# Kernel tuning notes

Hardware: AMD Instinct MI355X
Metric: run time of the kernel (lower is better)

The kernel has to match this reference:

```python
import jax, jax.numpy as jnp
import numpy as np

NH, DH = 16, 64          # n_head, d_head
CH = NH + DH             # 80
RQ, RK, RV = 6, 2, 2
ROPE_BASE = 10000.0


def _rotary(b, cache_len):
    # b: [B, T, R, DH]; rotates the d-factor exactly as the torch Rotary module
    T = b.shape[1]
    inv_freq = (1.0 / ROPE_BASE) ** (jnp.arange(0, DH, 2, dtype=jnp.float32) / DH)
    t = jnp.arange(T, dtype=jnp.float32) + cache_len
    freqs = jnp.outer(t, inv_freq)                      # [T, DH/2]
    cos = freqs[None, :, None, :].astype(b.dtype)
    sin = jnp.sin(freqs)[None, :, None, :].astype(b.dtype)
    cos = jnp.cos(freqs)[None, :, None, :].astype(b.dtype)
    x1, x2 = jnp.split(b, 2, axis=3)
    return jnp.concatenate([x1 * cos + x2 * sin, -x1 * sin + x2 * cos], axis=3)


def setup_inputs() -> dict:
    key = jax.random.key(0)
    k1, k2, k3, k4 = jax.random.split(key, 4)
    B, T, D = 2, 2048, 1024
    x = jax.random.normal(k1, (B, T, D), dtype=jnp.float32)
    # xavier-uniform-like scale for factor projections
    s_q = float(np.sqrt(6.0 / (D + CH)))
    s_o = float(np.sqrt(6.0 / (D + D)))
    W_abq = jax.random.uniform(k2, (RQ * CH, D), minval=-s_q, maxval=s_q, dtype=jnp.float32)
    W_abkv = jax.random.uniform(k3, ((RK + RV) * CH, D), minval=-s_q, maxval=s_q, dtype=jnp.float32)
    W_o = jax.random.uniform(k4, (D, D), minval=-s_o, maxval=s_o, dtype=jnp.float32)
    return {"x": x, "W_abq": W_abq, "W_abkv": W_abkv, "W_o": W_o}


def reference(x, W_abq, W_abkv, W_o):
    B, T, D = x.shape
    # low-rank factor projections
    abq = (x @ W_abq.T).reshape(B, T, RQ, CH)
    a_q, b_q = abq[..., :NH], abq[..., NH:]            # [B,T,RQ,NH], [B,T,RQ,DH]
    abkv = (x @ W_abkv.T).reshape(B, T, RK + RV, CH)
    a_kv = abkv[..., :NH]
    b_kv = _rotary(abkv[..., NH:], cache_len=0)        # RoPE applied to K/V d-factors only
    a_k, b_k = a_kv[:, :, :RK], b_kv[:, :, :RK]
    a_v, b_v = a_kv[:, :, RK:], b_kv[:, :, RK:]
    # tensor-product reconstruction of Q/K/V
    q = jnp.einsum('btrh,btrd->bthd', a_q, b_q) / RQ
    k = jnp.einsum('btrh,btrd->bthd', a_k, b_k) / RK
    v = jnp.einsum('btrh,btrd->bthd', a_v, b_v) / RV
    # causal attention (flex_attention default scale = 1/sqrt(dh))
    scale = 1.0 / jnp.sqrt(jnp.asarray(DH, dtype=q.dtype))
    scores = jnp.einsum('bqhd,bkhd->bhqk', q, k) * scale
    causal = jnp.tril(jnp.ones((T, T), dtype=bool))
    scores = jnp.where(causal[None, None], scores, jnp.finfo(scores.dtype).min)
    attn = jax.nn.softmax(scores, axis=-1)
    y = jnp.einsum('bhqk,bkhd->bqhd', attn, v).reshape(B, T, D)
    return y @ W_o.T
```

## Files before the change

### kernel.cpp

```cpp
#include <hip/hip_runtime.h>
#include <hip/hip_bf16.h>
#include <math.h>

#define NHEADS 16
#define DHEAD  64
#define CHDIM  80
#define RQn    6
#define RKn    2
#define RVn    2
#define BB     2
#define TT     2048
#define DDim   1024
#define NQK    800

using frag16 = __attribute__((ext_vector_type(8))) short;
using f32x4  = __attribute__((ext_vector_type(4))) float;
using f32x16 = __attribute__((ext_vector_type(16))) float;
using uint2v = __attribute__((ext_vector_type(2))) unsigned int;

#define AS1(p) ((const __attribute__((address_space(1))) unsigned int*)(p))
#define AS3(p) ((__attribute__((address_space(3))) unsigned int*)(p))

static __device__ __forceinline__ unsigned short bf16_bits(float f) {
    __hip_bfloat16 h = __float2bfloat16(f);
    return *(unsigned short*)&h;
}
static __device__ __forceinline__ unsigned int pk2(float a, float b) {
    return ((unsigned int)bf16_bits(b) << 16) | (unsigned int)bf16_bits(a);
}
static __device__ __forceinline__ float bfu2f(unsigned short u) {
    return __uint_as_float(((unsigned int)u) << 16);
}
static __device__ __forceinline__ float exp2_hw(float x) {
    return __builtin_amdgcn_exp2f(x);
}

__global__ __launch_bounds__(256) void cvt_all(
    const float* __restrict__ x, const float* __restrict__ wq,
    const float* __restrict__ wk, const float* __restrict__ wo,
    __hip_bfloat16* __restrict__ xb, __hip_bfloat16* __restrict__ wqk,
    __hip_bfloat16* __restrict__ wob)
{
    int bid = blockIdx.x;
    const float* src; __hip_bfloat16* dst; int n4;
    if (bid < 4096)      { src = x;  dst = xb;            n4 = 1048576; }
    else if (bid < 4576) { bid -= 4096; src = wq; dst = wqk;           n4 = 122880; }
    else if (bid < 4896) { bid -= 4576; src = wk; dst = wqk + 491520;  n4 = 81920; }
    else                 { bid -= 4896; src = wo; dst = wob;           n4 = 262144; }
    int i = bid * 256 + threadIdx.x;
    if (i < n4) {
        float4 v = *(const float4*)&src[i * 4];
        ushort4 o;
        o.x = bf16_bits(v.x); o.y = bf16_bits(v.y);
        o.z = bf16_bits(v.z); o.w = bf16_bits(v.w);
        *(ushort4*)&dst[i * 4] = o;
    }
}

template <bool BF16OUT>
__global__ __launch_bounds__(256) void gemm_bf16(
    const __hip_bfloat16* __restrict__ A, const __hip_bfloat16* __restrict__ W,
    void* __restrict__ Cv, int M, int N, int K)
{
    __shared__ __hip_bfloat16 Asl[2][64 * 64];
    __shared__ __hip_bfloat16 Bsl[2][128 * 64];
    const int tid = threadIdx.x;
    const int w = tid >> 6, lane = tid & 63;
    const int l16 = lane & 15, quad = lane >> 4;
    const int bm = blockIdx.y * 64, bn = blockIdx.x * 128;

    int rSA[2], cSA[2];
    #pragma unroll
    for (int j = 0; j < 2; j++) {
        int L = (w * 2 + j) * 64 + lane;
        rSA[j] = L >> 3;
        cSA[j] = (L & 7) ^ (rSA[j] & 7);
    }
    int rSB[4], cSB[4];
    #pragma unroll
    for (int j = 0; j < 4; j++) {
        int L = (w * 4 + j) * 64 + lane;
        int r = L >> 3;
        cSB[j] = (L & 7) ^ (r & 7);
        int rb = bn + r;
        rSB[j] = (rb < N) ? rb : (N - 1);
    }

    f32x4 acc[4][2];
    #pragma unroll
    for (int mt = 0; mt < 4; mt++)
        #pragma unroll
        for (int nt = 0; nt < 2; nt++)
            acc[mt][nt] = (f32x4){0.f, 0.f, 0.f, 0.f};

    const int nK = K >> 6;
    #pragma unroll
    for (int j = 0; j < 2; j++)
        __builtin_amdgcn_global_load_lds(AS1(A + (size_t)(bm + rSA[j]) * K + cSA[j] * 8),
                                         AS3(&Asl[0][(w * 2 + j) * 512]), 16, 0, 0);
    #pragma unroll
    for (int j = 0; j < 4; j++)
        __builtin_amdgcn_global_load_lds(AS1(W + (size_t)rSB[j] * K + cSB[j] * 8),
                                         AS3(&Bsl[0][(w * 4 + j) * 512]), 16, 0, 0);

    for (int kk = 0; kk < nK; kk++) {
        const int cur = kk & 1;
        __syncthreads();
        if (kk + 1 < nK) {
            const int k1 = (kk + 1) * 64;
            #pragma unroll
            for (int j = 0; j < 2; j++)
                __builtin_amdgcn_global_load_lds(AS1(A + (size_t)(bm + rSA[j]) * K + k1 + cSA[j] * 8),
                                                 AS3(&Asl[cur ^ 1][(w * 2 + j) * 512]), 16, 0, 0);
            #pragma unroll
            for (int j = 0; j < 4; j++)
                __builtin_amdgcn_global_load_lds(AS1(W + (size_t)rSB[j] * K + k1 + cSB[j] * 8),
                                                 AS3(&Bsl[cur ^ 1][(w * 4 + j) * 512]), 16, 0, 0);
        }
        #pragma unroll
        for (int ks = 0; ks < 2; ks++) {
            frag16 af[4], bf[2];
            #pragma unroll
            for (int mt = 0; mt < 4; mt++) {
                int r = mt * 16 + l16;
                af[mt] = *(const frag16*)&Asl[cur][r * 64 + (((ks * 4 + quad) ^ (r & 7)) * 8)];
            }
            #pragma unroll
            for (int nt = 0; nt < 2; nt++) {
                int r = w * 32 + nt * 16 + l16;
                bf[nt] = *(const frag16*)&Bsl[cur][r * 64 + (((ks * 4 + quad) ^ (r & 7)) * 8)];
            }
            #pragma unroll
            for (int mt = 0; mt < 4; mt++)
                #pragma unroll
                for (int nt = 0; nt < 2; nt++)
                    acc[mt][nt] = __builtin_amdgcn_mfma_f32_16x16x32_bf16(af[mt], bf[nt], acc[mt][nt], 0, 0, 0);
        }
    }
    #pragma unroll
    for (int mt = 0; mt < 4; mt++) {
        #pragma unroll
        for (int reg = 0; reg < 4; reg++) {
            int row = bm + mt * 16 + quad * 4 + reg;
            #pragma unroll
            for (int nt = 0; nt < 2; nt++) {
                int col = bn + w * 32 + nt * 16 + l16;
                if (col < N) {
                    if constexpr (BF16OUT)
                        ((__hip_bfloat16*)Cv)[(size_t)row * N + col] = __float2bfloat16(acc[mt][nt][reg]);
                    else
                        ((float*)Cv)[(size_t)row * N + col] = acc[mt][nt][reg];
                }
            }
        }
    }
}

__global__ __launch_bounds__(256) void qkv_kernel(
    const __hip_bfloat16* __restrict__ ab,
    __hip_bfloat16* __restrict__ q, __hip_bfloat16* __restrict__ k,
    __hip_bfloat16* __restrict__ vT)
{
    const int tok0 = blockIdx.x * 4;
    const int w = threadIdx.x >> 6;
    const int d = threadIdx.x & 63;
    const int token = tok0 + w;
    const int b = token / TT;
    const int t = token % TT;
    __shared__ float sab[4][NQK];
    __shared__ __align__(8) __hip_bfloat16 vbuf[NHEADS][DHEAD][4];
    const __hip_bfloat16* aq = ab + (size_t)token * NQK;
    #pragma unroll
    for (int i2 = d; i2 < NQK / 2; i2 += 64) {
        unsigned int u = *(const unsigned int*)&aq[i2 * 2];
        sab[w][i2 * 2 + 0] = bfu2f((unsigned short)(u & 0xffff));
        sab[w][i2 * 2 + 1] = bfu2f((unsigned short)(u >> 16));
    }
    const float* sq  = sab[w];
    const float* skv = sab[w] + 480;
    const int i32 = d & 31;
    float inv_freq = exp2_hw(-(float)i32 * (13.287712379549449f / 32.0f));
    float fr = (float)t * inv_freq;
    float c = cosf(fr), s = sinf(fr);
    __syncthreads();
    float rot[4];
    #pragma unroll
    for (int r = 0; r < 4; r++) {
        float x1 = skv[r * CHDIM + NHEADS + i32];
        float x2 = skv[r * CHDIM + NHEADS + 32 + i32];
        rot[r] = (d < 32) ? (x1 * c + x2 * s) : (-x1 * s + x2 * c);
    }
    float bqv[RQn];
    #pragma unroll
    for (int r = 0; r < RQn; r++) bqv[r] = sq[r * CHDIM + NHEADS + d];
    #pragma unroll
    for (int h = 0; h < NHEADS; h++) {
        float accq = 0.0f;
        #pragma unroll
        for (int r = 0; r < RQn; r++)
            accq += sq[r * CHDIM + h] * bqv[r];
        q[((size_t)(b * NHEADS + h) * TT + t) * DHEAD + d] =
            __float2bfloat16(accq * (0.125f / 6.0f) * 1.4426950408889634f);
        float acck = 0.0f, accv = 0.0f;
        #pragma unroll
        for (int r = 0; r < RKn; r++)
            acck += skv[r * CHDIM + h] * rot[r];
        #pragma unroll
        for (int r = 0; r < RVn; r++)
            accv += skv[(RKn + r) * CHDIM + h] * rot[RKn + r];
        k[((size_t)(b * NHEADS + h) * TT + t) * DHEAD + d] = __float2bfloat16(acck * 0.5f);
        vbuf[h][d][w] = __float2bfloat16(accv * 0.5f);
    }
    __syncthreads();
    const int t0 = tok0 % TT;
    const int b0 = tok0 / TT;
    for (int row = threadIdx.x; row < NHEADS * DHEAD; row += 256) {
        int h = row >> 6, dd = row & 63;
        *(uint2*)&vT[((size_t)(b0 * NHEADS + h) * DHEAD + dd) * TT + t0] =
            *(const uint2*)&vbuf[h][dd][0];
    }
}

static __device__ __forceinline__ void build_pfrag(
    const float* s0, const float* s1, frag16 Pf[4])
{
    #pragma unroll
    for (int k2 = 0; k2 < 4; k2++) {
        const float* sF = (k2 >= 2) ? s1 : s0;
        const int bs = 8 * (k2 & 1);
        unsigned int a0 = pk2(sF[bs + 0], sF[bs + 1]);
        unsigned int b0 = pk2(sF[bs + 2], sF[bs + 3]);
        unsigned int a1 = pk2(sF[bs + 4], sF[bs + 5]);
        unsigned int b1 = pk2(sF[bs + 6], sF[bs + 7]);
        uint2v ra = __builtin_amdgcn_permlane32_swap(a0, a1, false, false);
        uint2v rb = __builtin_amdgcn_permlane32_swap(b0, b1, false, false);
        union { frag16 f; unsigned int u[4]; } pf;
        pf.u[0] = ra[0]; pf.u[1] = rb[0]; pf.u[2] = ra[1]; pf.u[3] = rb[1];
        Pf[k2] = pf.f;
    }
}

static __device__ __forceinline__ void attn_tile(
    const __hip_bfloat16* __restrict__ Kc, const __hip_bfloat16* __restrict__ Vc,
    const frag16 qB[4], f32x16& O0, f32x16& O1, float& lpart,
    const int l31, const int hi, const int xi,
    const bool domask, const int kb0, const int qlane)
{
    f32x16 ST0 = {}, ST1 = {};
    __builtin_amdgcn_s_setprio(1);
    #pragma unroll
    for (int kt4 = 0; kt4 < 4; kt4++) {
        int c8 = kt4 * 2 + hi;
        frag16 kf0 = *(const frag16*)&Kc[l31 * 64 + ((c8 ^ xi) * 8)];
        frag16 kf1 = *(const frag16*)&Kc[(32 + l31) * 64 + ((c8 ^ xi) * 8)];
        ST0 = __builtin_amdgcn_mfma_f32_32x32x16_bf16(kf0, qB[kt4], ST0, 0, 0, 0);
        ST1 = __builtin_amdgcn_mfma_f32_32x32x16_bf16(kf1, qB[kt4], ST1, 0, 0, 0);
    }
    __builtin_amdgcn_s_setprio(0);
    float* s0 = (float*)&ST0;
    float* s1 = (float*)&ST1;
    if (domask) {
        int kbq = kb0 + 4 * hi;
        #pragma unroll
        for (int reg = 0; reg < 16; reg++) {
            int rowc = (reg & 3) + 8 * (reg >> 2);
            if (kbq + rowc > qlane)      s0[reg] = -1e30f;
            if (kbq + 32 + rowc > qlane) s1[reg] = -1e30f;
        }
    }
    #pragma unroll
    for (int reg = 0; reg < 16; reg++) {
        float p0 = exp2_hw(s0[reg]);
        float p1 = exp2_hw(s1[reg]);
        s0[reg] = p0; s1[reg] = p1;
        lpart += p0 + p1;
    }
    frag16 Pf[4];
    build_pfrag(s0, s1, Pf);
    __builtin_amdgcn_s_setprio(1);
    #pragma unroll
    for (int k2 = 0; k2 < 4; k2++) {
        int c8 = k2 * 2 + hi;
        frag16 vf0 = *(const frag16*)&Vc[l31 * 64 + ((c8 ^ xi) * 8)];
        frag16 vf1 = *(const frag16*)&Vc[(32 + l31) * 64 + ((c8 ^ xi) * 8)];
        O0 = __builtin_amdgcn_mfma_f32_32x32x16_bf16(vf0, Pf[k2], O0, 0, 0, 0);
        O1 = __builtin_amdgcn_mfma_f32_32x32x16_bf16(vf1, Pf[k2], O1, 0, 0, 0);
    }
    __builtin_amdgcn_s_setprio(0);
}

__global__ __launch_bounds__(256, 4) void flash_mfma(
    const __hip_bfloat16* __restrict__ q, const __hip_bfloat16* __restrict__ k,
    const __hip_bfloat16* __restrict__ vT,
    float* __restrict__ Op, float* __restrict__ Lp)
{
    const int Bid = blockIdx.x;
    const int m  = Bid & 255;
    const int g  = Bid >> 8;
    const int xcd = m & 7;
    const int bh  = xcd * 4 + ((m >> 3) & 3);
    const int i8  = m >> 5;
    const int qtoff = i8 >> 1;
    const int part  = i8 & 1;
    const int qt = (g == 0) ? (15 - qtoff) : (g == 1) ? qtoff
                 : (g == 2) ? (11 - qtoff) : (4 + qtoff);
    const int nst = qt + 1;
    const int k0  = part * nst;

    const int tid = threadIdx.x;
    const int w = tid >> 6;
    const int lane = tid & 63;
    const int l31 = lane & 31;
    const int hi = lane >> 5;
    const int xi = l31 & 7;
    const int paddr = (lane ^ 32) << 2;

    __shared__ __align__(16) __hip_bfloat16 KsF[2][4096];
    __shared__ __align__(16) __hip_bfloat16 VsF[2][4096];

    const size_t base = (size_t)bh * TT * DHEAD;
    const __hip_bfloat16* qb = q + base;
    const __hip_bfloat16* kb = k + base;
    const __hip_bfloat16* vb = vT + base;

    const int ktd = 2 * qt + (w >> 1);
    const int qlane = qt * 128 + w * 32 + l31;

    int offK[2], offV[2];
    #pragma unroll
    for (int j = 0; j < 2; j++) {
        int Lc = w * 128 + j * 64 + lane;
        int r = Lc >> 3, c8 = Lc & 7, g8 = c8 ^ (r & 7);
        offK[j] = r * 64 + g8 * 8;
        offV[j] = r * TT + g8 * 8;
    }

    frag16 qB[4];
    #pragma unroll
    for (int kt4 = 0; kt4 < 4; kt4++)
        qB[kt4] = *(const frag16*)&qb[(size_t)qlane * DHEAD + kt4 * 16 + hi * 8];

    f32x16 O0 = {}, O1 = {};
    float l = 0.0f;

    #pragma unroll
    for (int j = 0; j < 2; j++) {
        __builtin_amdgcn_global_load_lds(AS1(kb + (size_t)k0 * 4096 + offK[j]),
                                         AS3(&KsF[0][w * 1024 + j * 512]), 16, 0, 0);
        __builtin_amdgcn_global_load_lds(AS1(vb + (size_t)k0 * 64 + offV[j]),
                                         AS3(&VsF[0][w * 1024 + j * 512]), 16, 0, 0);
    }

    for (int kt = 0; kt < nst; kt++) {
        const int cur = kt & 1;
        __syncthreads();
        if (kt + 1 < nst) {
            const int phys1 = k0 + kt + 1;
            #pragma unroll
            for (int j = 0; j < 2; j++) {
                __builtin_amdgcn_global_load_lds(AS1(kb + (size_t)phys1 * 4096 + offK[j]),
                                                 AS3(&KsF[cur ^ 1][w * 1024 + j * 512]), 16, 0, 0);
                __builtin_amdgcn_global_load_lds(AS1(vb + (size_t)phys1 * 64 + offV[j]),
                                                 AS3(&VsF[cur ^ 1][w * 1024 + j * 512]), 16, 0, 0);
            }
        }
        const int phys = k0 + kt;
        if (phys <= ktd)
            attn_tile(KsF[cur], VsF[cur], qB, O0, O1, l, l31, hi, xi,
                      phys == ktd, phys * 64, qlane);
    }

    float lother = __int_as_float(__builtin_amdgcn_ds_bpermute(paddr, __float_as_int(l)));
    float ltot = l + lother;
    const int slot = bh * 16 + qt;
    const int rloc = w * 32 + l31;
    float* Od = Op + ((size_t)part * 512 + slot) * 8192 + (size_t)rloc * 64;
    float* o0 = (float*)&O0;
    float* o1 = (float*)&O1;
    #pragma unroll
    for (int gg = 0; gg < 4; gg++) {
        int d0 = 8 * gg + 4 * hi;
        *(float4*)&Od[d0]      = (float4){o0[4*gg+0], o0[4*gg+1], o0[4*gg+2], o0[4*gg+3]};
        *(float4*)&Od[32 + d0] = (float4){o1[4*gg+0], o1[4*gg+1], o1[4*gg+2], o1[4*gg+3]};
    }
    if (hi == 0) Lp[part * 65536 + slot * 128 + rloc] = ltot;
}

__global__ __launch_bounds__(256) void combine(
    const float* __restrict__ Op, const float* __restrict__ Lp,
    __hip_bfloat16* __restrict__ y)
{
    int idx = blockIdx.x * 256 + threadIdx.x;
    int cg = (idx & 7) * 8;
    int rowslot = idx >> 3;
    int slot = rowslot >> 7, row = rowslot & 127;
    int bh = slot >> 4, qt = slot & 15;
    int b = bh >> 4, h = bh & 15;
    int qrow = qt * 128 + row;
    float l0 = Lp[slot * 128 + row];
    float l1 = Lp[65536 + slot * 128 + row];
    float inv = 1.0f / (l0 + l1);
    const float* p0 = Op + (size_t)rowslot * 64 + cg;
    const float* p1 = p0 + 4194304;
    __hip_bfloat16* yp = y + ((size_t)(b * TT + qrow)) * DDim + h * DHEAD + cg;
    float4 a0 = *(const float4*)&p0[0];
    float4 a1 = *(const float4*)&p0[4];
    float4 b0 = *(const float4*)&p1[0];
    float4 b1 = *(const float4*)&p1[4];
    uint4 o;
    o.x = pk2((a0.x + b0.x) * inv, (a0.y + b0.y) * inv);
    o.y = pk2((a0.z + b0.z) * inv, (a0.w + b0.w) * inv);
    o.z = pk2((a1.x + b1.x) * inv, (a1.y + b1.y) * inv);
    o.w = pk2((a1.z + b1.z) * inv, (a1.w + b1.w) * inv);
    *(uint4*)&yp[0] = o;
}

extern "C" void kernel_launch(void* const* d_in, const int* in_sizes, int n_in,
                              void* d_out, int out_size, void* d_ws, size_t ws_size,
                              hipStream_t stream) {
    const float* x      = (const float*)d_in[0];
    const float* W_abq  = (const float*)d_in[1];
    const float* W_abkv = (const float*)d_in[2];
    const float* W_o    = (const float*)d_in[3];
    float* out = (float*)d_out;

    char* ws = (char*)d_ws;
    __hip_bfloat16* xb   = (__hip_bfloat16*)ws;  ws += (size_t)4194304 * 2;
    __hip_bfloat16* wqk  = (__hip_bfloat16*)ws;  ws += (size_t)NQK * 1024 * 2;
    __hip_bfloat16* wo_b = (__hip_bfloat16*)ws;  ws += (size_t)1048576 * 2;
    __hip_bfloat16* abqkv = (__hip_bfloat16*)ws; ws += (size_t)4096 * NQK * 2;
    __hip_bfloat16* qb = (__hip_bfloat16*)ws;    ws += (size_t)4194304 * 2;
    __hip_bfloat16* kb = (__hip_bfloat16*)ws;    ws += (size_t)4194304 * 2;
    __hip_bfloat16* vT = (__hip_bfloat16*)ws;    ws += (size_t)4194304 * 2;
    __hip_bfloat16* yb = (__hip_bfloat16*)ws;    ws += (size_t)4194304 * 2;
    float* Op = (float*)ws;                      ws += (size_t)2 * 4194304 * 4;
    float* Lp = (float*)ws;                      ws += (size_t)2 * 65536 * 4;

    cvt_all<<<dim3(5920), dim3(256), 0, stream>>>(x, W_abq, W_abkv, W_o, xb, wqk, wo_b);
    gemm_bf16<true><<<dim3(7, 64), dim3(256), 0, stream>>>(xb, wqk, abqkv, 4096, NQK, 1024);
    qkv_kernel<<<dim3(1024), dim3(256), 0, stream>>>(abqkv, qb, kb, vT);
    flash_mfma<<<dim3(1024), dim3(256), 0, stream>>>(qb, kb, vT, Op, Lp);
    combine<<<dim3(2048), dim3(256), 0, stream>>>(Op, Lp, yb);
    gemm_bf16<false><<<dim3(8, 64), dim3(256), 0, stream>>>(yb, wo_b, out, 4096, 1024, 1024);
}
```

Before: 166.5 us.

## Split flash attention into single-wave blocks loading K/V fragments directly from global

The flash attention kernel drops its shared-memory double-buffered K/V staging. Each 64-thread block is now one wave that loads its own K and V MFMA fragments straight from global memory into registers. The grid grows from 1024 to 4096 blocks, and each wave skips key tiles beyond its causal diagonal instead of iterating and syncing with the other waves. This removes the __syncthreads barriers and LDS traffic, at the cost of four times redundant global/L2 reads of K/V across waves and no prefetch overlap.

```diff
diff --git a/kernel.cpp b/kernel.cpp
--- a/kernel.cpp
+++ b/kernel.cpp
@@ -240,21 +240,33 @@
     }
 }
 
-static __device__ __forceinline__ void attn_tile(
-    const __hip_bfloat16* __restrict__ Kc, const __hip_bfloat16* __restrict__ Vc,
+static __device__ __forceinline__ void attn_tile_direct(
+    const __hip_bfloat16* __restrict__ Kt,
+    const __hip_bfloat16* __restrict__ Vt,
     const frag16 qB[4], f32x16& O0, f32x16& O1, float& lpart,
-    const int l31, const int hi, const int xi,
+    const int l31, const int hi,
     const bool domask, const int kb0, const int qlane)
 {
+    frag16 kf0[4], kf1[4];
+    #pragma unroll
+    for (int kt4 = 0; kt4 < 4; kt4++) {
+        const int c8 = kt4 * 2 + hi;
+        kf0[kt4] = *(const frag16*)&Kt[(size_t)l31 * 64 + c8 * 8];
+        kf1[kt4] = *(const frag16*)&Kt[(size_t)(32 + l31) * 64 + c8 * 8];
+    }
+    frag16 vf0[4], vf1[4];
+    #pragma unroll
+    for (int k2 = 0; k2 < 4; k2++) {
+        const int c8 = k2 * 2 + hi;
+        vf0[k2] = *(const frag16*)&Vt[(size_t)l31 * TT + c8 * 8];
+        vf1[k2] = *(const frag16*)&Vt[(size_t)(32 + l31) * TT + c8 * 8];
+    }
     f32x16 ST0 = {}, ST1 = {};
     __builtin_amdgcn_s_setprio(1);
     #pragma unroll
     for (int kt4 = 0; kt4 < 4; kt4++) {
-        int c8 = kt4 * 2 + hi;
-        frag16 kf0 = *(const frag16*)&Kc[l31 * 64 + ((c8 ^ xi) * 8)];
-        frag16 kf1 = *(const frag16*)&Kc[(32 + l31) * 64 + ((c8 ^ xi) * 8)];
-        ST0 = __builtin_amdgcn_mfma_f32_32x32x16_bf16(kf0, qB[kt4], ST0, 0, 0, 0);
-        ST1 = __builtin_amdgcn_mfma_f32_32x32x16_bf16(kf1, qB[kt4], ST1, 0, 0, 0);
+        ST0 = __builtin_amdgcn_mfma_f32_32x32x16_bf16(kf0[kt4], qB[kt4], ST0, 0, 0, 0);
+        ST1 = __builtin_amdgcn_mfma_f32_32x32x16_bf16(kf1[kt4], qB[kt4], ST1, 0, 0, 0);
     }
     __builtin_amdgcn_s_setprio(0);
     float* s0 = (float*)&ST0;
@@ -280,23 +292,21 @@
     __builtin_amdgcn_s_setprio(1);
     #pragma unroll
     for (int k2 = 0; k2 < 4; k2++) {
-        int c8 = k2 * 2 + hi;
-        frag16 vf0 = *(const frag16*)&Vc[l31 * 64 + ((c8 ^ xi) * 8)];
-        frag16 vf1 = *(const frag16*)&Vc[(32 + l31) * 64 + ((c8 ^ xi) * 8)];
-        O0 = __builtin_amdgcn_mfma_f32_32x32x16_bf16(vf0, Pf[k2], O0, 0, 0, 0);
-        O1 = __builtin_amdgcn_mfma_f32_32x32x16_bf16(vf1, Pf[k2], O1, 0, 0, 0);
+        O0 = __builtin_amdgcn_mfma_f32_32x32x16_bf16(vf0[k2], Pf[k2], O0, 0, 0, 0);
+        O1 = __builtin_amdgcn_mfma_f32_32x32x16_bf16(vf1[k2], Pf[k2], O1, 0, 0, 0);
     }
     __builtin_amdgcn_s_setprio(0);
 }
 
-__global__ __launch_bounds__(256, 4) void flash_mfma(
+__global__ __launch_bounds__(64) void flash_mfma(
     const __hip_bfloat16* __restrict__ q, const __hip_bfloat16* __restrict__ k,
     const __hip_bfloat16* __restrict__ vT,
     float* __restrict__ Op, float* __restrict__ Lp)
 {
     const int Bid = blockIdx.x;
     const int m  = Bid & 255;
-    const int g  = Bid >> 8;
+    const int g  = (Bid >> 8) & 3;
+    const int w  = Bid >> 10;
     const int xcd = m & 7;
     const int bh  = xcd * 4 + ((m >> 3) & 3);
     const int i8  = m >> 5;
@@ -307,16 +317,10 @@
     const int nst = qt + 1;
     const int k0  = part * nst;
 
-    const int tid = threadIdx.x;
-    const int w = tid >> 6;
-    const int lane = tid & 63;
+    const int lane = threadIdx.x;
     const int l31 = lane & 31;
     const int hi = lane >> 5;
-    const int xi = l31 & 7;
     const int paddr = (lane ^ 32) << 2;
-
-    __shared__ __align__(16) __hip_bfloat16 KsF[2][4096];
-    __shared__ __align__(16) __hip_bfloat16 VsF[2][4096];
 
     const size_t base = (size_t)bh * TT * DHEAD;
     const __hip_bfloat16* qb = q + base;
@@ -325,15 +329,8 @@
 
     const int ktd = 2 * qt + (w >> 1);
     const int qlane = qt * 128 + w * 32 + l31;
-
-    int offK[2], offV[2];
-    #pragma unroll
-    for (int j = 0; j < 2; j++) {
-        int Lc = w * 128 + j * 64 + lane;
-        int r = Lc >> 3, c8 = Lc & 7, g8 = c8 ^ (r & 7);
-        offK[j] = r * 64 + g8 * 8;
-        offV[j] = r * TT + g8 * 8;
-    }
+    const int kend = k0 + nst;
+    const int pend = (kend < ktd + 1) ? kend : (ktd + 1);
 
     frag16 qB[4];
     #pragma unroll
@@ -343,31 +340,10 @@
     f32x16 O0 = {}, O1 = {};
     float l = 0.0f;
 
-    #pragma unroll
-    for (int j = 0; j < 2; j++) {
-        __builtin_amdgcn_global_load_lds(AS1(kb + (size_t)k0 * 4096 + offK[j]),
-                                         AS3(&KsF[0][w * 1024 + j * 512]), 16, 0, 0);
-        __builtin_amdgcn_global_load_lds(AS1(vb + (size_t)k0 * 64 + offV[j]),
-                                         AS3(&VsF[0][w * 1024 + j * 512]), 16, 0, 0);
-    }
-
-    for (int kt = 0; kt < nst; kt++) {
-        const int cur = kt & 1;
-        __syncthreads();
-        if (kt + 1 < nst) {
-            const int phys1 = k0 + kt + 1;
-            #pragma unroll
-            for (int j = 0; j < 2; j++) {
-                __builtin_amdgcn_global_load_lds(AS1(kb + (size_t)phys1 * 4096 + offK[j]),
-                                                 AS3(&KsF[cur ^ 1][w * 1024 + j * 512]), 16, 0, 0);
-                __builtin_amdgcn_global_load_lds(AS1(vb + (size_t)phys1 * 64 + offV[j]),
-                                                 AS3(&VsF[cur ^ 1][w * 1024 + j * 512]), 16, 0, 0);
-            }
-        }
-        const int phys = k0 + kt;
-        if (phys <= ktd)
-            attn_tile(KsF[cur], VsF[cur], qB, O0, O1, l, l31, hi, xi,
-                      phys == ktd, phys * 64, qlane);
+    for (int phys = k0; phys < pend; phys++) {
+        attn_tile_direct(kb + (size_t)phys * 64 * DHEAD, vb + (size_t)phys * 64,
+                         qB, O0, O1, l, l31, hi,
+                         phys == ktd, phys * 64, qlane);
     }
 
     float lother = __int_as_float(__builtin_amdgcn_ds_bpermute(paddr, __float_as_int(l)));
@@ -439,7 +415,7 @@
     cvt_all<<<dim3(5920), dim3(256), 0, stream>>>(x, W_abq, W_abkv, W_o, xb, wqk, wo_b);
     gemm_bf16<true><<<dim3(7, 64), dim3(256), 0, stream>>>(xb, wqk, abqkv, 4096, NQK, 1024);
     qkv_kernel<<<dim3(1024), dim3(256), 0, stream>>>(abqkv, qb, kb, vT);
-    flash_mfma<<<dim3(1024), dim3(256), 0, stream>>>(qb, kb, vT, Op, Lp);
+    flash_mfma<<<dim3(4096), dim3(64), 0, stream>>>(qb, kb, vT, Op, Lp);
     combine<<<dim3(2048), dim3(256), 0, stream>>>(Op, Lp, yb);
     gemm_bf16<false><<<dim3(8, 64), dim3(256), 0, stream>>>(yb, wo_b, out, 4096, 1024, 1024);
 }
```

Measured after the change: 210.2 us. +26.3%, slower.

## Merge split-K attention halves in one 512-thread block, drop combine kernel

Applied to the files above, without the earlier changes.

The two KV-split halves of each query tile now run as two 4-wave groups inside a single 512-thread block. Their partial outputs and row sums are merged through shared memory, normalized, and written directly as bf16. This removes the fp32 partial-output round trip through global memory and the separate combine launch. In exchange, LDS per block doubles to 64KB, the block size doubles, and an extra barrier plus LDS exchange is added at the end, which may reduce occupancy.

```diff
diff --git a/kernel.cpp b/kernel.cpp
--- a/kernel.cpp
+++ b/kernel.cpp
@@ -289,34 +289,33 @@
     __builtin_amdgcn_s_setprio(0);
 }
 
-__global__ __launch_bounds__(256, 4) void flash_mfma(
+__global__ __launch_bounds__(512, 4) void flash_mfma(
     const __hip_bfloat16* __restrict__ q, const __hip_bfloat16* __restrict__ k,
-    const __hip_bfloat16* __restrict__ vT,
-    float* __restrict__ Op, float* __restrict__ Lp)
+    const __hip_bfloat16* __restrict__ vT, __hip_bfloat16* __restrict__ y)
 {
     const int Bid = blockIdx.x;
-    const int m  = Bid & 255;
-    const int g  = Bid >> 8;
+    const int m = Bid & 255;
+    const int half = Bid >> 8;
     const int xcd = m & 7;
     const int bh  = xcd * 4 + ((m >> 3) & 3);
-    const int i8  = m >> 5;
-    const int qtoff = i8 >> 1;
-    const int part  = i8 & 1;
-    const int qt = (g == 0) ? (15 - qtoff) : (g == 1) ? qtoff
-                 : (g == 2) ? (11 - qtoff) : (4 + qtoff);
+    const int qx  = m >> 5;
+    const int qt  = half ? qx : (15 - qx);
     const int nst = qt + 1;
-    const int k0  = part * nst;
 
     const int tid = threadIdx.x;
-    const int w = tid >> 6;
+    const int w8 = tid >> 6;
+    const int part = w8 >> 2;
+    const int w = w8 & 3;
     const int lane = tid & 63;
     const int l31 = lane & 31;
     const int hi = lane >> 5;
     const int xi = l31 & 7;
     const int paddr = (lane ^ 32) << 2;
-
-    __shared__ __align__(16) __hip_bfloat16 KsF[2][4096];
-    __shared__ __align__(16) __hip_bfloat16 VsF[2][4096];
+    const int k0 = part * nst;
+
+    __shared__ __align__(16) char smem[65536];
+    __hip_bfloat16* Ks = (__hip_bfloat16*)(smem + part * 32768);
+    __hip_bfloat16* Vs = (__hip_bfloat16*)(smem + part * 32768 + 16384);
 
     const size_t base = (size_t)bh * TT * DHEAD;
     const __hip_bfloat16* qb = q + base;
@@ -346,9 +345,9 @@
     #pragma unroll
     for (int j = 0; j < 2; j++) {
         __builtin_amdgcn_global_load_lds(AS1(kb + (size_t)k0 * 4096 + offK[j]),
-                                         AS3(&KsF[0][w * 1024 + j * 512]), 16, 0, 0);
+                                         AS3(&Ks[w * 1024 + j * 512]), 16, 0, 0);
         __builtin_amdgcn_global_load_lds(AS1(vb + (size_t)k0 * 64 + offV[j]),
-                                         AS3(&VsF[0][w * 1024 + j * 512]), 16, 0, 0);
+                                         AS3(&Vs[w * 1024 + j * 512]), 16, 0, 0);
     }
 
     for (int kt = 0; kt < nst; kt++) {
@@ -359,60 +358,50 @@
             #pragma unroll
             for (int j = 0; j < 2; j++) {
                 __builtin_amdgcn_global_load_lds(AS1(kb + (size_t)phys1 * 4096 + offK[j]),
-                                                 AS3(&KsF[cur ^ 1][w * 1024 + j * 512]), 16, 0, 0);
+                                                 AS3(&Ks[(cur ^ 1) * 4096 + w * 1024 + j * 512]), 16, 0, 0);
                 __builtin_amdgcn_global_load_lds(AS1(vb + (size_t)phys1 * 64 + offV[j]),
-                                                 AS3(&VsF[cur ^ 1][w * 1024 + j * 512]), 16, 0, 0);
+                                                 AS3(&Vs[(cur ^ 1) * 4096 + w * 1024 + j * 512]), 16, 0, 0);
             }
         }
         const int phys = k0 + kt;
         if (phys <= ktd)
-            attn_tile(KsF[cur], VsF[cur], qB, O0, O1, l, l31, hi, xi,
-                      phys == ktd, phys * 64, qlane);
-    }
-
-    float lother = __int_as_float(__builtin_amdgcn_ds_bpermute(paddr, __float_as_int(l)));
-    float ltot = l + lother;
-    const int slot = bh * 16 + qt;
-    const int rloc = w * 32 + l31;
-    float* Od = Op + ((size_t)part * 512 + slot) * 8192 + (size_t)rloc * 64;
+            attn_tile(Ks + cur * 4096, Vs + cur * 4096, qB, O0, O1, l,
+                      l31, hi, xi, phys == ktd, phys * 64, qlane);
+    }
+
+    __syncthreads();
+    float* Oex = (float*)smem;
+    float* lex = (float*)(smem + 33792);
     float* o0 = (float*)&O0;
     float* o1 = (float*)&O1;
-    #pragma unroll
-    for (int gg = 0; gg < 4; gg++) {
-        int d0 = 8 * gg + 4 * hi;
-        *(float4*)&Od[d0]      = (float4){o0[4*gg+0], o0[4*gg+1], o0[4*gg+2], o0[4*gg+3]};
-        *(float4*)&Od[32 + d0] = (float4){o1[4*gg+0], o1[4*gg+1], o1[4*gg+2], o1[4*gg+3]};
-    }
-    if (hi == 0) Lp[part * 65536 + slot * 128 + rloc] = ltot;
-}
-
-__global__ __launch_bounds__(256) void combine(
-    const float* __restrict__ Op, const float* __restrict__ Lp,
-    __hip_bfloat16* __restrict__ y)
-{
-    int idx = blockIdx.x * 256 + threadIdx.x;
-    int cg = (idx & 7) * 8;
-    int rowslot = idx >> 3;
-    int slot = rowslot >> 7, row = rowslot & 127;
-    int bh = slot >> 4, qt = slot & 15;
-    int b = bh >> 4, h = bh & 15;
-    int qrow = qt * 128 + row;
-    float l0 = Lp[slot * 128 + row];
-    float l1 = Lp[65536 + slot * 128 + row];
-    float inv = 1.0f / (l0 + l1);
-    const float* p0 = Op + (size_t)rowslot * 64 + cg;
-    const float* p1 = p0 + 4194304;
-    __hip_bfloat16* yp = y + ((size_t)(b * TT + qrow)) * DDim + h * DHEAD + cg;
-    float4 a0 = *(const float4*)&p0[0];
-    float4 a1 = *(const float4*)&p0[4];
-    float4 b0 = *(const float4*)&p1[0];
-    float4 b1 = *(const float4*)&p1[4];
-    uint4 o;
-    o.x = pk2((a0.x + b0.x) * inv, (a0.y + b0.y) * inv);
-    o.y = pk2((a0.z + b0.z) * inv, (a0.w + b0.w) * inv);
-    o.z = pk2((a1.x + b1.x) * inv, (a1.y + b1.y) * inv);
-    o.w = pk2((a1.z + b1.z) * inv, (a1.w + b1.w) * inv);
-    *(uint4*)&yp[0] = o;
+    if (part == 1) {
+        float* dst = Oex + (w * 64 + lane) * 33;
+        #pragma unroll
+        for (int i = 0; i < 16; i++) { dst[i] = o0[i]; dst[16 + i] = o1[i]; }
+        lex[w * 64 + lane] = l;
+    }
+    __syncthreads();
+    if (part == 0) {
+        const float* src = Oex + (w * 64 + lane) * 33;
+        #pragma unroll
+        for (int i = 0; i < 16; i++) { o0[i] += src[i]; o1[i] += src[16 + i]; }
+        l += lex[w * 64 + lane];
+        float lother = __int_as_float(__builtin_amdgcn_ds_bpermute(paddr, __float_as_int(l)));
+        float inv = 1.0f / (l + lother);
+        const int b = bh >> 4, h = bh & 15;
+        __hip_bfloat16* yp = y + ((size_t)(b * TT + qlane)) * DDim + h * DHEAD;
+        #pragma unroll
+        for (int gg = 0; gg < 4; gg++) {
+            int d0 = 8 * gg + 4 * hi;
+            uint2 pa, pb;
+            pa.x = pk2(o0[4*gg+0] * inv, o0[4*gg+1] * inv);
+            pa.y = pk2(o0[4*gg+2] * inv, o0[4*gg+3] * inv);
+            pb.x = pk2(o1[4*gg+0] * inv, o1[4*gg+1] * inv);
+            pb.y = pk2(o1[4*gg+2] * inv, o1[4*gg+3] * inv);
+            *(uint2*)&yp[d0] = pa;
+            *(uint2*)&yp[32 + d0] = pb;
+        }
+    }
 }
 
 extern "C" void kernel_launch(void* const* d_in, const int* in_sizes, int n_in,
@@ -433,13 +422,10 @@
     __hip_bfloat16* kb = (__hip_bfloat16*)ws;    ws += (size_t)4194304 * 2;
     __hip_bfloat16* vT = (__hip_bfloat16*)ws;    ws += (size_t)4194304 * 2;
     __hip_bfloat16* yb = (__hip_bfloat16*)ws;    ws += (size_t)4194304 * 2;
-    float* Op = (float*)ws;                      ws += (size_t)2 * 4194304 * 4;
-    float* Lp = (float*)ws;                      ws += (size_t)2 * 65536 * 4;
 
     cvt_all<<<dim3(5920), dim3(256), 0, stream>>>(x, W_abq, W_abkv, W_o, xb, wqk, wo_b);
     gemm_bf16<true><<<dim3(7, 64), dim3(256), 0, stream>>>(xb, wqk, abqkv, 4096, NQK, 1024);
     qkv_kernel<<<dim3(1024), dim3(256), 0, stream>>>(abqkv, qb, kb, vT);
-    flash_mfma<<<dim3(1024), dim3(256), 0, stream>>>(qb, kb, vT, Op, Lp);
-    combine<<<dim3(2048), dim3(256), 0, stream>>>(Op, Lp, yb);
+    flash_mfma<<<dim3(512), dim3(512), 0, stream>>>(qb, kb, vT, yb);
     gemm_bf16<false><<<dim3(8, 64), dim3(256), 0, stream>>>(yb, wo_b, out, 4096, 1024, 1024);
 }
```

New measurement: 157.8 us. 1.05x faster.
